# Optimization experiments

Hardware: AMD Instinct MI355X
Metric: run time of the kernel (lower is better)

The kernel has to match this reference:

```python
import jax, jax.numpy as jnp
import numpy as np

T, B, EMBED, HEADS = 1024, 32, 512, 8
HEAD = EMBED // HEADS      # per-head value size (= head_dim = 64)
KEYD = 16                  # key_size hard-coded to 16 in MultiheadAttention
MEM_SLOTS, TOPK = 8, 3
NUM_GATES = 2 * EMBED      # gate_style='unit' -> 2*mem_size


def layer_norm(x, g, b, eps=1e-5):
    mu = jnp.mean(x, axis=-1, keepdims=True)
    var = jnp.var(x, axis=-1, keepdims=True)
    return (x - mu) * jax.lax.rsqrt(var + eps) * g + b


def mha(q_src, kv_src, Wq, bq, Wk, bk, Wv, bv, use_topk):
    # q from q_src (RelationalMemory passes 'memory' arg as query source),
    # k/v from kv_src ('input' arg). No 1/sqrt(d) scaling in original code.
    Bq, Sq = q_src.shape[0], q_src.shape[1]
    Sk = kv_src.shape[1]
    q = (q_src @ Wq + bq).reshape(Bq, Sq, HEADS, KEYD)
    k = (kv_src @ Wk + bk).reshape(Bq, Sk, HEADS, KEYD)
    v = (kv_src @ Wv + bv).reshape(Bq, Sk, HEADS, HEAD)
    probs = jax.nn.softmax(jnp.einsum('bqhd,bkhd->bhqk', q, k), axis=-1)
    if use_topk:
        _, idx = jax.lax.top_k(probs, TOPK)  # (B,H,Sq,TOPK)
        mask = jnp.sum(jax.nn.one_hot(idx, Sk, dtype=probs.dtype), axis=-2)
        probs = probs * mask  # post-softmax top-k gate (scatter of ones)
    out = jnp.einsum('bhqk,bkhd->bqhd', probs, v)
    return out.reshape(Bq, Sq, EMBED)


def setup_inputs() -> dict:
    rng = jax.random.key(0)
    ks = jax.random.split(rng, 12)

    def n(k, shape, s=0.02):
        return jax.random.normal(k, shape, dtype=jnp.float32) * s

    # initial_state: eye(mem_slots) zero-padded to mem_size, per batch element
    mem0 = jnp.pad(jnp.eye(MEM_SLOTS, dtype=jnp.float32), ((0, 0), (0, EMBED - MEM_SLOTS)))
    return {
        'query': jax.random.normal(ks[0], (T, B, EMBED), jnp.float32),
        'key': jax.random.normal(ks[1], (T, B, EMBED), jnp.float32),
        'memory': jnp.tile(mem0[None], (B, 1, 1)),
        'W_in': n(ks[2], (EMBED, EMBED)), 'b_in': jnp.zeros((EMBED,), jnp.float32),
        'Wq': n(ks[3], (EMBED, KEYD * HEADS)), 'bq': jnp.zeros((KEYD * HEADS,), jnp.float32),
        'Wk': n(ks[4], (EMBED, KEYD * HEADS)), 'bk': jnp.zeros((KEYD * HEADS,), jnp.float32),
        'Wv': n(ks[5], (EMBED, EMBED)), 'bv': jnp.zeros((EMBED,), jnp.float32),
        'W_mlp': n(ks[6], (EMBED, EMBED)), 'b_mlp': jnp.zeros((EMBED,), jnp.float32),
        'g1': jnp.ones((EMBED,), jnp.float32), 'be1': jnp.zeros((EMBED,), jnp.float32),
        'g2': jnp.ones((EMBED,), jnp.float32), 'be2': jnp.zeros((EMBED,), jnp.float32),
        'w_rep': jax.random.normal(ks[7], (EMBED,), jnp.float32),
        'W_ig': n(ks[8], (EMBED, NUM_GATES)), 'b_ig': jnp.zeros((NUM_GATES,), jnp.float32),
        'W_mg': n(ks[9], (MEM_SLOTS, EMBED, NUM_GATES)), 'b_mg': jnp.zeros((MEM_SLOTS, NUM_GATES), jnp.float32),
        'forget_bias': jnp.asarray(1.0, jnp.float32),
        'input_bias': jnp.asarray(0.0, jnp.float32),
    }


def reference(query, key, memory, W_in, b_in, Wq, bq, Wk, bk, Wv, bv,
              W_mlp, b_mlp, g1, be1, g2, be2, w_rep, W_ig, b_ig,
              W_mg, b_mg, forget_bias, input_bias):
    # query only shape-checked by the torch module; key carries the content
    inputs = jnp.transpose(key, (1, 0, 2))          # (B, T, E)
    x = inputs @ W_in + b_in                        # input_projector
    # attend_over_memory (num_blocks=1): memory slots query the tokens, top-k write
    attended = mha(memory, x, Wq, bq, Wk, bk, Wv, bv, use_topk=True)
    m = layer_norm(memory + attended, g1, be1)
    mlp = jax.nn.relu(m @ W_mlp + b_mlp)            # attention_mlp_layers=1
    new_mem = layer_norm(m + mlp, g2, be2)
    # gating (gate_style='unit')
    gi = jnp.mean(jax.nn.relu(w_rep * x), axis=1) @ W_ig + b_ig      # RepeatLinear -> (B, 2E)
    gm = jnp.einsum('bsm,smn->bsn', jnp.tanh(memory), W_mg) + b_mg   # GroupLinearLayer -> (B, S, 2E)
    in_g, f_g = jnp.split(gi[:, None, :] + gm, 2, axis=-1)
    in_g = jax.nn.sigmoid(in_g + input_bias)
    f_g = jax.nn.sigmoid(f_g + forget_bias)
    new_mem = in_g * jnp.tanh(new_mem) + f_g * memory
    # broadcast read: every token queries the updated memory (no top-k)
    hx = mha(x, new_mem, Wq, bq, Wk, bk, Wv, bv, use_topk=False)     # (B, T, E)
    return jnp.transpose(hx, (1, 0, 2))             # (T, B, E) as in torch forward
```

## Files before the change

### kernel.cpp

```cpp
#include <hip/hip_runtime.h>
#include <stdint.h>

typedef unsigned short u16;
typedef __bf16 bf16x8 __attribute__((ext_vector_type(8)));
typedef float f32x4 __attribute__((ext_vector_type(4)));


__device__ __forceinline__ u16 f2b(float f) {
  union { __bf16 h; u16 u; } v; v.h = (__bf16)f; return v.u;
}
__device__ __forceinline__ float b2f(u16 h) {
  union { uint32_t u; float f; } v; v.u = ((uint32_t)h) << 16; return v.f;
}
__device__ __forceinline__ void gload_lds16(const void* g, void* l) {
  __builtin_amdgcn_global_load_lds(
      (const __attribute__((address_space(1))) unsigned int*)g,
      (__attribute__((address_space(3))) unsigned int*)l, 16, 0, 0);
}

__global__ void k_prep(const float* __restrict__ W_in, u16* __restrict__ WxT,
                       const float* __restrict__ Wv, u16* __restrict__ WvT,
                       const float* __restrict__ mem, float* __restrict__ tm,
                       const float* __restrict__ b_in, float* __restrict__ bfull,
                       const float* __restrict__ Wk, const float* __restrict__ Wq,
                       u16* __restrict__ WkqTr, u16* __restrict__ WinB,
                       const float* __restrict__ W_mlp, u16* __restrict__ WmlpT,
                       const float* __restrict__ key, u16* __restrict__ keyB) {
  int idx = blockIdx.x * 256 + threadIdx.x;
  if (idx < 262144) {
    int k = idx >> 9, n = idx & 511;
    WxT[n * 512 + k] = f2b(W_in[idx]);
  } else if (idx < 524288) {
    int j = idx - 262144;
    int k = j >> 9, n = j & 511;
    WvT[n * 512 + k] = f2b(Wv[j]);
  } else if (idx < 655360) {
    int j = idx - 524288;
    tm[j] = tanhf(mem[j]);
  } else if (idx < 655872) {
    int j = idx - 655360;
    bfull[j] = b_in[j];
  } else if (idx < 786944) {
    int i = idx - 655872;
    int j = i >> 9, n = i & 511;
    WkqTr[i] = f2b(j < 128 ? Wk[n * 128 + j] : Wq[n * 128 + j - 128]);
  } else if (idx < 1049088) {
    int i = idx - 786944;
    WinB[i] = f2b(W_in[i]);
  } else if (idx < 1311232) {
    int i = idx - 1049088;
    int k = i >> 9, n = i & 511;
    WmlpT[n * 512 + k] = f2b(W_mlp[i]);
  } else {
    int i = idx - 1311232;
    int r = i >> 6, e8 = i & 63;
    int b = r >> 10, t = r & 1023;
    const float* src = key + ((size_t)(t * 32 + b) << 9) + e8 * 8;
    float4 lo = *(const float4*)src;
    float4 hi = *(const float4*)(src + 4);
    bf16x8 o;
    o[0] = (__bf16)lo.x; o[1] = (__bf16)lo.y; o[2] = (__bf16)lo.z; o[3] = (__bf16)lo.w;
    o[4] = (__bf16)hi.x; o[5] = (__bf16)hi.y; o[6] = (__bf16)hi.z; o[7] = (__bf16)hi.w;
    *(bf16x8*)(keyB + ((size_t)r << 9) + e8 * 8) = o;
  }
}

__global__ __launch_bounds__(256) void k_wprep2(
    const u16* __restrict__ A, const u16* __restrict__ Bt, u16* __restrict__ WxT,
    const float* __restrict__ b_in, const float* __restrict__ Wk, const float* __restrict__ Wq,
    const float* __restrict__ bk, const float* __restrict__ bq, float* __restrict__ bfull,
    const float* __restrict__ memory, const float* __restrict__ bqf, float* __restrict__ qm)
{
  const int bid = blockIdx.x;
  const int tid = threadIdx.x;
  if (bid < 8) {
    __shared__ u16 As[128 * 32];
    __shared__ u16 Bs[128 * 32];
    const int m0 = (bid & 1) * 128;
    const int n0 = (bid >> 1) * 128;
    const int lane = tid & 63;
    const int wid = tid >> 6;
    const int wm = (wid >> 1) * 64;
    const int wn = (wid & 1) * 64;
    f32x4 acc[4][4];
    #pragma unroll
    for (int i = 0; i < 4; ++i)
      #pragma unroll
      for (int j = 0; j < 4; ++j) acc[i][j] = (f32x4){0.f, 0.f, 0.f, 0.f};
    for (int kt = 0; kt < 16; ++kt) {
      const int k0 = kt << 5;
      __syncthreads();
      #pragma unroll
      for (int c = 0; c < 2; ++c) {
        int o = c * 2048 + tid * 8;
        int row = o >> 5, ck = o & 31;
        gload_lds16(A + (size_t)(m0 + row) * 512 + k0 + ck, As + o);
        gload_lds16(Bt + (size_t)(n0 + row) * 512 + k0 + ck, Bs + o);
      }
      __syncthreads();
      const int r = lane & 15;
      const int kb = (lane >> 4) * 8;
      bf16x8 af[4], bfr[4];
      #pragma unroll
      for (int i = 0; i < 4; ++i) {
        af[i]  = *(const bf16x8*)(As + (wm + i * 16 + r) * 32 + kb);
        bfr[i] = *(const bf16x8*)(Bs + (wn + i * 16 + r) * 32 + kb);
      }
      #pragma unroll
      for (int i = 0; i < 4; ++i)
        #pragma unroll
        for (int j = 0; j < 4; ++j)
          acc[i][j] = __builtin_amdgcn_mfma_f32_16x16x32_bf16(af[i], bfr[j], acc[i][j], 0, 0, 0);
    }
    const int cl = lane & 15;
    const int rl = (lane >> 4) * 4;
    #pragma unroll
    for (int j = 0; j < 4; ++j) {
      const int col = n0 + wn + j * 16 + cl;
      #pragma unroll
      for (int i = 0; i < 4; ++i) {
        #pragma unroll
        for (int rr = 0; rr < 4; ++rr) {
          const int row = m0 + wm + i * 16 + rl + rr;
          WxT[(size_t)(512 + row) * 512 + col] = f2b(acc[i][j][rr]);
        }
      }
    }
  } else if (bid == 8) {
    __shared__ float bs[512];
    const int j = tid;
    bs[tid] = b_in[tid];
    bs[256 + tid] = b_in[256 + tid];
    __syncthreads();
    const float* W = (j < 128) ? (Wk + j) : (Wq + j - 128);
    float a = 0.f;
    #pragma unroll 8
    for (int n = 0; n < 512; ++n)
      a += bs[n] * W[(size_t)n * 128];
    bfull[512 + j] = a + ((j < 128) ? bk[j] : bq[j - 128]);
  } else {
    const int bs_ = bid - 9;
    const int b = bs_ >> 3, s = bs_ & 7;
    const int col = tid & 127, half = tid >> 7;
    __shared__ float mrow[512];
    __shared__ float part[2][128];
    *(float2*)&mrow[tid * 2] = *(const float2*)&memory[(size_t)(b * 8 + s) * 512 + tid * 2];
    __syncthreads();
    float a = 0.f;
    const int e0 = half * 256;
    for (int e = 0; e < 256; ++e)
      a += mrow[e0 + e] * Wq[(size_t)(e0 + e) * 128 + col];
    part[half][col] = a;
    __syncthreads();
    if (tid < 128)
      qm[(size_t)(b * 8 + s) * 128 + tid] = part[0][tid] + part[1][tid] + bqf[tid];
  }
}

__global__ __launch_bounds__(256) void gemm_xkq(
    const u16* __restrict__ keyB, const u16* __restrict__ Bt,
    const float* __restrict__ bias, u16* __restrict__ x, u16* __restrict__ kq)
{
  __shared__ u16 smem[16384];
  u16* As = smem;
  u16* Bs = smem + 8192;
  const int tid = threadIdx.x;
  const int bid = blockIdx.x;
  const int wgid = (bid & 7) * 192 + (bid >> 3);
  const int m0 = (wgid / 6) * 128;
  const int n0 = (wgid % 6) * 128;
  const int lane = tid & 63;
  const int wid = tid >> 6;
  const int wm = (wid >> 1) * 64;
  const int wn = (wid & 1) * 64;

  f32x4 acc[4][4];
  #pragma unroll
  for (int i = 0; i < 4; ++i)
    #pragma unroll
    for (int j = 0; j < 4; ++j) acc[i][j] = (f32x4){0.f, 0.f, 0.f, 0.f};

  for (int kt = 0; kt < 8; ++kt) {
    const int k0 = kt << 6;
    __syncthreads();
    #pragma unroll
    for (int c = 0; c < 4; ++c) {
      const int q = c * 256 + tid;
      const int row = q >> 3;
      const int c8 = q & 7;
      const int lc = c8 ^ (row & 7);
      gload_lds16(keyB + (size_t)(m0 + row) * 512 + k0 + lc * 8, As + q * 8);
      gload_lds16(Bt   + (size_t)(n0 + row) * 512 + k0 + lc * 8, Bs + q * 8);
    }
    __syncthreads();
    const int r = lane & 15;
    const int hi = lane >> 4;
    bf16x8 af[4][2], bfr[4][2];
    #pragma unroll
    for (int i = 0; i < 4; ++i) {
      const int ra = wm + i * 16 + r;
      const int rb = wn + i * 16 + r;
      #pragma unroll
      for (int kk = 0; kk < 2; ++kk) {
        af[i][kk]  = *(const bf16x8*)(As + ra * 64 + (((kk * 4 + hi)) ^ (ra & 7)) * 8);
        bfr[i][kk] = *(const bf16x8*)(Bs + rb * 64 + (((kk * 4 + hi)) ^ (rb & 7)) * 8);
      }
    }
    #pragma unroll
    for (int kk = 0; kk < 2; ++kk)
      #pragma unroll
      for (int i = 0; i < 4; ++i)
        #pragma unroll
        for (int j = 0; j < 4; ++j)
          acc[i][j] = __builtin_amdgcn_mfma_f32_16x16x32_bf16(af[i][kk], bfr[j][kk], acc[i][j], 0, 0, 0);
  }
  __syncthreads();
  u16* Cs = smem;
  const int cl = lane & 15;
  const int rl = (lane >> 4) * 4;
  #pragma unroll
  for (int j = 0; j < 4; ++j) {
    const int lcol = wn + j * 16 + cl;
    const float bsv = bias[n0 + lcol];
    #pragma unroll
    for (int i = 0; i < 4; ++i)
      #pragma unroll
      for (int rr = 0; rr < 4; ++rr)
        Cs[(wm + i * 16 + rl + rr) * 128 + lcol] = f2b(acc[i][j][rr] + bsv);
  }
  __syncthreads();
  #pragma unroll
  for (int c = 0; c < 8; ++c) {
    const int chunk = c * 256 + tid;
    const int row = chunk >> 4, c8 = chunk & 15;
    uint4 v = *(const uint4*)&Cs[row * 128 + c8 * 8];
    if (n0 < 512)
      *(uint4*)(x + (size_t)(m0 + row) * 512 + n0 + c8 * 8) = v;
    else
      *(uint4*)(kq + (size_t)(m0 + row) * 256 + (n0 - 512) + c8 * 8) = v;
  }
}

__global__ __launch_bounds__(256) void k_scores_topk(
    const float* __restrict__ qm, const u16* __restrict__ kq,
    const u16* __restrict__ x, float* __restrict__ p3, u16* __restrict__ XW)
{
  const int b = blockIdx.x, h = blockIdx.y, s = blockIdx.z;
  const int tid = threadIdx.x;
  __shared__ float swv[4];
  __shared__ int   swi[4];
  __shared__ float ssv[4];

  float q[16];
  const float* qp = qm + ((size_t)(b * 8 + s) * 128 + h * 16);
  #pragma unroll
  for (int d = 0; d < 16; ++d) q[d] = qp[d];

  float sc[4];
  #pragma unroll
  for (int j = 0; j < 4; ++j) {
    const int t = j * 256 + tid;
    const u16* kr = kq + ((size_t)(b * 1024 + t)) * 256 + h * 16;
    uint4 v0 = *(const uint4*)kr;
    uint4 v1 = *(const uint4*)(kr + 8);
    const u16* p0 = (const u16*)&v0;
    const u16* p1 = (const u16*)&v1;
    float a = 0.f;
    #pragma unroll
    for (int d = 0; d < 8; ++d) a += q[d] * b2f(p0[d]);
    #pragma unroll
    for (int d = 0; d < 8; ++d) a += q[8 + d] * b2f(p1[d]);
    sc[j] = a;
  }

  int   seli[3];
  float selv[3];
  float ssum = 0.f;
  #pragma unroll
  for (int pass = 0; pass < 3; ++pass) {
    float bv_ = -1e30f; int bi_ = 1 << 30;
    #pragma unroll
    for (int j = 0; j < 4; ++j) {
      const int t = j * 256 + tid;
      bool skip = false;
      for (int k = 0; k < pass; ++k) skip |= (t == seli[k]);
      float v = skip ? -1e30f : sc[j];
      if (v > bv_ || (v == bv_ && t < bi_)) { bv_ = v; bi_ = t; }
    }
    #pragma unroll
    for (int o = 32; o > 0; o >>= 1) {
      float ov = __shfl_xor(bv_, o);
      int   oi = __shfl_xor(bi_, o);
      if (ov > bv_ || (ov == bv_ && oi < bi_)) { bv_ = ov; bi_ = oi; }
    }
    __syncthreads();
    if ((tid & 63) == 0) { swv[tid >> 6] = bv_; swi[tid >> 6] = bi_; }
    __syncthreads();
    float wv = swv[0]; int wi = swi[0];
    #pragma unroll
    for (int w = 1; w < 4; ++w) {
      float ov = swv[w]; int oi = swi[w];
      if (ov > wv || (ov == wv && oi < wi)) { wv = ov; wi = oi; }
    }
    selv[pass] = wv; seli[pass] = wi;

    if (pass == 0) {
      float se = 0.f;
      #pragma unroll
      for (int j = 0; j < 4; ++j) se += __expf(sc[j] - wv);
      #pragma unroll
      for (int o = 32; o > 0; o >>= 1) se += __shfl_xor(se, o);
      __syncthreads();
      if ((tid & 63) == 0) ssv[tid >> 6] = se;
      __syncthreads();
      ssum = ssv[0] + ssv[1] + ssv[2] + ssv[3];
    }
  }

  const float m0v = selv[0];
  const float inv = 1.f / ssum;
  const float p0 = __expf(selv[0] - m0v) * inv;
  const float p1 = __expf(selv[1] - m0v) * inv;
  const float p2 = __expf(selv[2] - m0v) * inv;
  if (tid == 0) {
    const size_t base = (size_t)(b * 64 + h * 8 + s);
    p3[base * 4 + 0] = p0;
    p3[base * 4 + 1] = p1;
    p3[base * 4 + 2] = p2;
    p3[base * 4 + 3] = p0 + p1 + p2;
  }
  if (tid < 64) {
    const u16* xb = x + ((size_t)b << 19) + tid * 8;
    uint4 a0 = *(const uint4*)(xb + ((size_t)seli[0] << 9));
    uint4 a1 = *(const uint4*)(xb + ((size_t)seli[1] << 9));
    uint4 a2 = *(const uint4*)(xb + ((size_t)seli[2] << 9));
    const u16* e0 = (const u16*)&a0;
    const u16* e1 = (const u16*)&a1;
    const u16* e2 = (const u16*)&a2;
    u16 ov[8];
    #pragma unroll
    for (int k = 0; k < 8; ++k)
      ov[k] = f2b(p0 * b2f(e0[k]) + p1 * b2f(e1[k]) + p2 * b2f(e2[k]));
    *(uint4*)(XW + (size_t)h * 131072 + (size_t)(b * 8 + s) * 512 + tid * 8) = *(const uint4*)ov;
  }
}

__global__ __launch_bounds__(256) void k_attgi(
    const u16* __restrict__ XW, const u16* __restrict__ WvT,
    const float* __restrict__ p3, const float* __restrict__ bvv,
    float* __restrict__ att,
    const u16* __restrict__ x, const float* __restrict__ w_rep,
    float* __restrict__ gpart)
{
  __shared__ u16 As[128 * 32];
  __shared__ u16 Bs[64 * 32];
  __shared__ float ps[4][512];
  const int bid = blockIdx.x;
  const int tid = threadIdx.x;
  if (bid < 16) {
    const int h = bid >> 1;
    const int m0 = (bid & 1) * 128;
    const int lane = tid & 63;
    const int wid = tid >> 6;
    const int wm = wid * 32;
    const u16* A = XW + (size_t)h * 131072;
    const u16* Bh = WvT + (size_t)h * 64 * 512;

    f32x4 acc[2][4];
    #pragma unroll
    for (int i = 0; i < 2; ++i)
      #pragma unroll
      for (int j = 0; j < 4; ++j) acc[i][j] = (f32x4){0.f, 0.f, 0.f, 0.f};

    for (int kt = 0; kt < 16; ++kt) {
      const int k0 = kt << 5;
      __syncthreads();
      #pragma unroll
      for (int c = 0; c < 2; ++c) {
        int o = c * 2048 + tid * 8;
        int row = o >> 5, ck = o & 31;
        gload_lds16(A + (size_t)(m0 + row) * 512 + k0 + ck, As + o);
      }
      {
        int row = tid >> 2, ck = (tid & 3) * 8;
        gload_lds16(Bh + (size_t)row * 512 + k0 + ck, Bs + row * 32 + ck);
      }
      __syncthreads();
      const int r = lane & 15;
      const int kb = (lane >> 4) * 8;
      bf16x8 af[2], bfr[4];
      #pragma unroll
      for (int i = 0; i < 2; ++i)
        af[i] = *(const bf16x8*)(As + (wm + i * 16 + r) * 32 + kb);
      #pragma unroll
      for (int j = 0; j < 4; ++j)
        bfr[j] = *(const bf16x8*)(Bs + (j * 16 + r) * 32 + kb);
      #pragma unroll
      for (int i = 0; i < 2; ++i)
        #pragma unroll
        for (int j = 0; j < 4; ++j)
          acc[i][j] = __builtin_amdgcn_mfma_f32_16x16x32_bf16(af[i], bfr[j], acc[i][j], 0, 0, 0);
    }
    const int cl = lane & 15;
    const int rl = (lane >> 4) * 4;
    #pragma unroll
    for (int i = 0; i < 2; ++i) {
      #pragma unroll
      for (int rr = 0; rr < 4; ++rr) {
        const int row = m0 + wm + i * 16 + rl + rr;
        const int bb = row >> 3, ss = row & 7;
        const float sp = p3[(size_t)(bb * 64 + h * 8 + ss) * 4 + 3];
        #pragma unroll
        for (int j = 0; j < 4; ++j) {
          const int col = h * 64 + j * 16 + cl;
          att[(size_t)row * 512 + col] = acc[i][j][rr] + sp * bvv[col];
        }
      }
    }
  } else {
    const int j = bid - 16;
    const int b = j >> 3, ch = j & 7;
    const int e8 = tid & 63, tp = tid >> 6;
    float w[8], acc[8];
    #pragma unroll
    for (int k = 0; k < 8; ++k) { w[k] = w_rep[e8 * 8 + k]; acc[k] = 0.f; }
    const int t0 = ch * 128 + tp * 32;
    for (int tt = 0; tt < 32; ++tt) {
      uint4 v = *(const uint4*)(x + ((size_t)(b * 1024 + t0 + tt) << 9) + e8 * 8);
      const u16* pv = (const u16*)&v;
      #pragma unroll
      for (int k = 0; k < 8; ++k) acc[k] += fmaxf(w[k] * b2f(pv[k]), 0.f);
    }
    #pragma unroll
    for (int k = 0; k < 8; ++k) ps[tp][e8 * 8 + k] = acc[k];
    __syncthreads();
    #pragma unroll
    for (int r = 0; r < 2; ++r) {
      int e = r * 256 + tid;
      gpart[(size_t)(b * 8 + ch) * 512 + e] = ps[0][e] + ps[1][e] + ps[2][e] + ps[3][e];
    }
  }
}

__global__ __launch_bounds__(256) void k_ln1(
    const float* __restrict__ memory, const float* __restrict__ att,
    const float* __restrict__ g1, const float* __restrict__ be1,
    float* __restrict__ m_f32, u16* __restrict__ m_bf)
{
  const int b = blockIdx.x, s = blockIdx.y;
  const int tid = threadIdx.x;
  __shared__ float r1[256], r2[256];
  const size_t base = (size_t)(b * 8 + s) * 512;
  float v0 = memory[base + tid] + att[base + tid];
  float v1 = memory[base + 256 + tid] + att[base + 256 + tid];
  r1[tid] = v0 + v1; r2[tid] = v0 * v0 + v1 * v1;
  __syncthreads();
  for (int off = 128; off > 0; off >>= 1) {
    if (tid < off) { r1[tid] += r1[tid + off]; r2[tid] += r2[tid + off]; }
    __syncthreads();
  }
  float mu = r1[0] * (1.f / 512.f);
  float var = r2[0] * (1.f / 512.f) - mu * mu;
  float rs = rsqrtf(var + 1e-5f);
  float m0v = (v0 - mu) * rs * g1[tid] + be1[tid];
  float m1v = (v1 - mu) * rs * g1[tid + 256] + be1[tid + 256];
  m_f32[base + tid] = m0v;
  m_f32[base + 256 + tid] = m1v;
  m_bf[base + tid] = f2b(m0v);
  m_bf[base + 256 + tid] = f2b(m1v);
}

__global__ __launch_bounds__(256) void k_mlpgigm(
    const u16* __restrict__ A, const u16* __restrict__ Bt,
    const float* __restrict__ b_mlp, const float* __restrict__ m_f32,
    float* __restrict__ hbuf,
    const float* __restrict__ tm, const float* __restrict__ W_mg, float* __restrict__ gmp,
    const float* __restrict__ gpart, const float* __restrict__ W_ig,
    const float* __restrict__ b_ig, float* __restrict__ gip)
{
  __shared__ __align__(16) char smem[73728];
  const int bid = blockIdx.x;
  const int tid = threadIdx.x;
  if (bid < 8) {
    u16* As = (u16*)smem;
    u16* Bs = (u16*)(smem + 16384);
    const int m0 = (bid >> 2) * 128;
    const int n0 = (bid & 3) * 128;
    const int lane = tid & 63;
    const int wid = tid >> 6;
    const int wm = (wid >> 1) * 64;
    const int wn = (wid & 1) * 64;

    f32x4 acc[4][4];
    #pragma unroll
    for (int i = 0; i < 4; ++i)
      #pragma unroll
      for (int j = 0; j < 4; ++j) acc[i][j] = (f32x4){0.f, 0.f, 0.f, 0.f};

    for (int kt = 0; kt < 8; ++kt) {
      const int k0 = kt << 6;
      __syncthreads();
      #pragma unroll
      for (int c = 0; c < 4; ++c) {
        const int q = c * 256 + tid;
        const int row = q >> 3;
        const int c8 = q & 7;
        const int lc = c8 ^ (row & 7);
        gload_lds16(A  + (size_t)(m0 + row) * 512 + k0 + lc * 8, As + q * 8);
        gload_lds16(Bt + (size_t)(n0 + row) * 512 + k0 + lc * 8, Bs + q * 8);
      }
      __syncthreads();
      const int r = lane & 15;
      const int hi = lane >> 4;
      bf16x8 af[4][2], bfr[4][2];
      #pragma unroll
      for (int i = 0; i < 4; ++i) {
        const int ra = wm + i * 16 + r;
        const int rb = wn + i * 16 + r;
        #pragma unroll
        for (int kk = 0; kk < 2; ++kk) {
          af[i][kk]  = *(const bf16x8*)(As + ra * 64 + (((kk * 4 + hi)) ^ (ra & 7)) * 8);
          bfr[i][kk] = *(const bf16x8*)(Bs + rb * 64 + (((kk * 4 + hi)) ^ (rb & 7)) * 8);
        }
      }
      #pragma unroll
      for (int kk = 0; kk < 2; ++kk)
        #pragma unroll
        for (int i = 0; i < 4; ++i)
          #pragma unroll
          for (int j = 0; j < 4; ++j)
            acc[i][j] = __builtin_amdgcn_mfma_f32_16x16x32_bf16(af[i][kk], bfr[j][kk], acc[i][j], 0, 0, 0);
    }
    const int cl = lane & 15;
    const int rl = (lane >> 4) * 4;
    #pragma unroll
    for (int j = 0; j < 4; ++j) {
      const int col = n0 + wn + j * 16 + cl;
      const float bsv = b_mlp[col];
      #pragma unroll
      for (int i = 0; i < 4; ++i) {
        #pragma unroll
        for (int rr = 0; rr < 4; ++rr) {
          const int row = m0 + wm + i * 16 + rl + rr;
          hbuf[(size_t)row * 512 + col] = m_f32[(size_t)row * 512 + col] + fmaxf(acc[i][j][rr] + bsv, 0.f);
        }
      }
    }
  } else if (bid < 264) {
    float* wtile = (float*)smem;
    float* vals  = (float*)(smem + 65536);
    const int g = bid - 8;
    const int s = g >> 5, nc = (g >> 3) & 3, kc = g & 7;
    const int k0 = kc * 64;
    const float* wsrc = W_mg + (size_t)s * 524288 + (size_t)k0 * 1024 + nc * 256;
    #pragma unroll
    for (int i = 0; i < 16; ++i) {
      const int q = i * 256 + tid;
      const int row = q >> 6, c16 = q & 63;
      gload_lds16(wsrc + (size_t)row * 1024 + c16 * 4, wtile + q * 4);
    }
    {
      int i = tid * 2;
      int b = i >> 4, k4 = i & 15;
      *(float4*)&vals[b * 64 + k4 * 4] = *(const float4*)&tm[(size_t)(b * 8 + s) * 512 + k0 + k4 * 4];
      i++;
      b = i >> 4; k4 = i & 15;
      *(float4*)&vals[b * 64 + k4 * 4] = *(const float4*)&tm[(size_t)(b * 8 + s) * 512 + k0 + k4 * 4];
    }
    __syncthreads();
    const int col = nc * 256 + tid;
    float acc[32];
    #pragma unroll
    for (int b = 0; b < 32; ++b) acc[b] = 0.f;
    for (int kk = 0; kk < 64; ++kk) {
      float w = wtile[kk * 256 + tid];
      #pragma unroll
      for (int b = 0; b < 32; ++b) acc[b] += vals[b * 64 + kk] * w;
    }
    #pragma unroll
    for (int b = 0; b < 32; ++b)
      gmp[(size_t)((kc * 32 + b) * 8 + s) * 1024 + col] = acc[b];
  } else {
    float* wtile = (float*)smem;
    float* vals  = (float*)(smem + 65536);
    const int j = bid - 264;
    const int nc = j >> 3, kc = j & 7;
    const int k0 = kc * 64;
    const float* wsrc = W_ig + (size_t)k0 * 1024 + nc * 256;
    #pragma unroll
    for (int i = 0; i < 16; ++i) {
      const int q = i * 256 + tid;
      const int row = q >> 6, c16 = q & 63;
      gload_lds16(wsrc + (size_t)row * 1024 + c16 * 4, wtile + q * 4);
    }
    #pragma unroll
    for (int i = 0; i < 8; ++i) {
      const int idx = i * 256 + tid;
      const int b = idx >> 6, k = idx & 63;
      float a = 0.f;
      #pragma unroll
      for (int ch = 0; ch < 8; ++ch)
        a += gpart[(size_t)(b * 8 + ch) * 512 + k0 + k];
      vals[b * 64 + k] = a * (1.f / 1024.f);
    }
    __syncthreads();
    const int col = nc * 256 + tid;
    float acc[32];
    #pragma unroll
    for (int b = 0; b < 32; ++b) acc[b] = 0.f;
    for (int kk = 0; kk < 64; ++kk) {
      float w = wtile[kk * 256 + tid];
      #pragma unroll
      for (int b = 0; b < 32; ++b) acc[b] += vals[b * 64 + kk] * w;
    }
    const float badd = (kc == 0) ? b_ig[col] : 0.f;
    #pragma unroll
    for (int b = 0; b < 32; ++b)
      gip[(size_t)(kc * 32 + b) * 1024 + col] = acc[b] + badd;
  }
}

__global__ __launch_bounds__(256) void k_ln2gate(
    const float* __restrict__ hbuf, const float* __restrict__ g2, const float* __restrict__ be2,
    const float* __restrict__ gip, const float* __restrict__ gmp,
    const float* __restrict__ b_mg, const float* __restrict__ memory,
    const float* __restrict__ fbias, const float* __restrict__ ibias,
    float* __restrict__ nmem)
{
  const int b = blockIdx.x, s = blockIdx.y;
  const int tid = threadIdx.x;
  __shared__ float r1[256], r2[256];
  const size_t base = (size_t)(b * 8 + s) * 512;
  float v0 = hbuf[base + tid];
  float v1 = hbuf[base + 256 + tid];
  r1[tid] = v0 + v1; r2[tid] = v0 * v0 + v1 * v1;
  __syncthreads();
  for (int off = 128; off > 0; off >>= 1) {
    if (tid < off) { r1[tid] += r1[tid + off]; r2[tid] += r2[tid + off]; }
    __syncthreads();
  }
  float mu = r1[0] * (1.f / 512.f);
  float var = r2[0] * (1.f / 512.f) - mu * mu;
  float rs = rsqrtf(var + 1e-5f);
  const float fb = fbias[0], ib = ibias[0];
  #pragma unroll
  for (int rr = 0; rr < 2; ++rr) {
    const int e = rr * 256 + tid;
    const float v = (rr == 0) ? v0 : v1;
    float ln = (v - mu) * rs * g2[e] + be2[e];
    float gin = b_mg[s * 1024 + e], gfn = b_mg[s * 1024 + 512 + e];
    #pragma unroll
    for (int kc = 0; kc < 8; ++kc) {
      size_t gp = (size_t)((kc * 32 + b) * 8 + s) * 1024;
      gin += gmp[gp + e];
      gfn += gmp[gp + 512 + e];
    }
    float giv_i = 0.f, giv_f = 0.f;
    #pragma unroll
    for (int kc = 0; kc < 8; ++kc) {
      size_t gp = (size_t)(kc * 32 + b) * 1024;
      giv_i += gip[gp + e];
      giv_f += gip[gp + 512 + e];
    }
    float ing = 1.f / (1.f + __expf(-(giv_i + gin + ib)));
    float fg  = 1.f / (1.f + __expf(-(giv_f + gfn + fb)));
    nmem[base + e] = ing * tanhf(ln) + fg * memory[base + e];
  }
}

__global__ __launch_bounds__(256) void k_kv_part(
    const float* __restrict__ nmem, const float* __restrict__ Wk, const float* __restrict__ Wv,
    float* __restrict__ kvp)
{
  const int b = blockIdx.x, nc = blockIdx.y, kc = blockIdx.z;
  const int tid = threadIdx.x;
  const int col = tid & 127, rg = tid >> 7;
  const int k0 = kc * 128;
  __shared__ float nm[8][128];
  {
    int s = tid >> 5, k4 = tid & 31;
    *(float4*)&nm[s][k4 * 4] = *(const float4*)&nmem[(size_t)(b * 8 + s) * 512 + k0 + k4 * 4];
  }
  __syncthreads();
  const int cg = nc * 128 + col;
  const float* wp; int stride;
  if (nc == 0) { wp = Wk + (size_t)k0 * 128 + cg; stride = 128; }
  else         { wp = Wv + (size_t)k0 * 512 + (cg - 128); stride = 512; }
  const int b0 = rg * 4;
  float a0 = 0.f, a1 = 0.f, a2 = 0.f, a3 = 0.f;
  #pragma unroll 4
  for (int kk = 0; kk < 128; ++kk) {
    float w = wp[(size_t)kk * stride];
    a0 += nm[b0][kk] * w;
    a1 += nm[b0 + 1][kk] * w;
    a2 += nm[b0 + 2][kk] * w;
    a3 += nm[b0 + 3][kk] * w;
  }
  kvp[(size_t)((kc * 32 + b) * 8 + b0    ) * 640 + cg] = a0;
  kvp[(size_t)((kc * 32 + b) * 8 + b0 + 1) * 640 + cg] = a1;
  kvp[(size_t)((kc * 32 + b) * 8 + b0 + 2) * 640 + cg] = a2;
  kvp[(size_t)((kc * 32 + b) * 8 + b0 + 3) * 640 + cg] = a3;
}

__global__ __launch_bounds__(256) void k_out_attn(
    const u16* __restrict__ kq, const float* __restrict__ kvp,
    const float* __restrict__ bk, const float* __restrict__ bv,
    float* __restrict__ out)
{
  int b = blockIdx.x, tc = blockIdx.y;
  int tid = threadIdx.x;
  __shared__ float km[1024];
  __shared__ float vm[4096];
  __shared__ float pr[1024];
  for (int i = tid; i < 1024; i += 256) {
    int s = i >> 7, j = i & 127;
    float a = bk[j];
    #pragma unroll
    for (int kc = 0; kc < 4; ++kc)
      a += kvp[(size_t)((kc * 32 + b) * 8 + s) * 640 + j];
    km[i] = a;
  }
  for (int i = tid; i < 4096; i += 256) {
    int s = i >> 9, c = i & 511;
    float a = bv[c];
    #pragma unroll
    for (int kc = 0; kc < 4; ++kc)
      a += kvp[(size_t)((kc * 32 + b) * 8 + s) * 640 + 128 + c];
    vm[i] = a;
  }
  __syncthreads();
  if (tid < 128) {
    int tt = tid >> 3, hh = tid & 7;
    int t = tc * 16 + tt;
    const u16* qrow = kq + ((size_t)(b * 1024 + t)) * 256 + 128 + hh * 16;
    float q[16];
    #pragma unroll
    for (int d = 0; d < 16; ++d) q[d] = b2f(qrow[d]);
    float s8[8]; float mx = -1e38f;
    #pragma unroll
    for (int s = 0; s < 8; ++s) {
      float a = 0.f;
      #pragma unroll
      for (int d = 0; d < 16; ++d) a += q[d] * km[s * 128 + hh * 16 + d];
      s8[s] = a; mx = fmaxf(mx, a);
    }
    float se = 0.f;
    #pragma unroll
    for (int s = 0; s < 8; ++s) { s8[s] = __expf(s8[s] - mx); se += s8[s]; }
    float inv = 1.f / se;
    #pragma unroll
    for (int s = 0; s < 8; ++s) pr[(tt * 8 + hh) * 8 + s] = s8[s] * inv;
  }
  __syncthreads();
  #pragma unroll
  for (int oi = 0; oi < 8; ++oi) {
    int o = oi * 256 + tid;
    int tt = o >> 7, c4 = o & 127;
    int c = c4 * 4, hh = c >> 6;
    const float* prp = &pr[(tt * 8 + hh) * 8];
    float4 r = {0.f, 0.f, 0.f, 0.f};
    #pragma unroll
    for (int s = 0; s < 8; ++s) {
      float p = prp[s];
      float4 v = *(const float4*)&vm[s * 512 + c];
      r.x += p * v.x; r.y += p * v.y; r.z += p * v.z; r.w += p * v.w;
    }
    int t = tc * 16 + tt;
    *(float4*)&out[((size_t)t * 32 + b) * 512 + c] = r;
  }
}

extern "C" void kernel_launch(void* const* d_in, const int* in_sizes, int n_in,
                              void* d_out, int out_size, void* d_ws, size_t ws_size,
                              hipStream_t stream) {
  (void)in_sizes; (void)n_in; (void)out_size; (void)ws_size;
  const float* key   = (const float*)d_in[1];
  const float* memory= (const float*)d_in[2];
  const float* W_in  = (const float*)d_in[3];
  const float* b_in  = (const float*)d_in[4];
  const float* Wq    = (const float*)d_in[5];
  const float* bq    = (const float*)d_in[6];
  const float* Wk    = (const float*)d_in[7];
  const float* bk    = (const float*)d_in[8];
  const float* Wv    = (const float*)d_in[9];
  const float* bv    = (const float*)d_in[10];
  const float* W_mlp = (const float*)d_in[11];
  const float* b_mlp = (const float*)d_in[12];
  const float* g1    = (const float*)d_in[13];
  const float* be1   = (const float*)d_in[14];
  const float* g2    = (const float*)d_in[15];
  const float* be2   = (const float*)d_in[16];
  const float* w_rep = (const float*)d_in[17];
  const float* W_ig  = (const float*)d_in[18];
  const float* b_ig  = (const float*)d_in[19];
  const float* W_mg  = (const float*)d_in[20];
  const float* b_mg  = (const float*)d_in[21];
  const float* fbias = (const float*)d_in[22];
  const float* ibias = (const float*)d_in[23];
  float* out = (float*)d_out;

  char* p = (char*)d_ws;
  auto alloc = [&](size_t bytes) { char* r = p; p += (bytes + 255) & ~(size_t)255; return r; };
  u16* x       = (u16*)alloc(33554432);
  u16* keyB    = (u16*)alloc(33554432);
  u16* kq      = (u16*)alloc(16777216);
  u16* WxT     = (u16*)alloc(786432);
  u16* WvT     = (u16*)alloc(524288);
  u16* WkqTr   = (u16*)alloc(262144);
  u16* WinB    = (u16*)alloc(524288);
  u16* WmlpT   = (u16*)alloc(524288);
  float* bfull = (float*)alloc(3072);
  float* gpart = (float*)alloc(524288);
  float* gip   = (float*)alloc(1048576);
  float* gmp   = (float*)alloc(8388608);
  float* att   = (float*)alloc(524288);
  float* m_f32 = (float*)alloc(524288);
  u16*   m_bf  = (u16*)alloc(262144);
  float* hbuf  = (float*)alloc(524288);
  float* nmem  = (float*)alloc(524288);
  float* kvp   = (float*)alloc(2621440);
  float* tm    = (float*)alloc(524288);
  float* qmw   = (float*)alloc(131072);
  float* p3    = (float*)alloc(32768);
  u16* XW      = (u16*)alloc(2097152);

  k_prep<<<13314, 256, 0, stream>>>(W_in, WxT, Wv, WvT, memory, tm, b_in, bfull,
                                    Wk, Wq, WkqTr, WinB, W_mlp, WmlpT, key, keyB);
  k_wprep2<<<265, 256, 0, stream>>>(WkqTr, WinB, WxT, b_in, Wk, Wq, bk, bq, bfull,
                                    memory, bq, qmw);
  gemm_xkq<<<1536, 256, 0, stream>>>(keyB, WxT, bfull, x, kq);
  k_scores_topk<<<dim3(32, 8, 8), 256, 0, stream>>>(qmw, kq, x, p3, XW);
  k_attgi<<<272, 256, 0, stream>>>(XW, WvT, p3, bv, att, x, w_rep, gpart);
  k_ln1<<<dim3(32, 8), 256, 0, stream>>>(memory, att, g1, be1, m_f32, m_bf);
  k_mlpgigm<<<296, 256, 0, stream>>>(m_bf, WmlpT, b_mlp, m_f32, hbuf,
                                     tm, W_mg, gmp, gpart, W_ig, b_ig, gip);
  k_ln2gate<<<dim3(32, 8), 256, 0, stream>>>(hbuf, g2, be2, gip, gmp, b_mg, memory,
                                             fbias, ibias, nmem);
  k_kv_part<<<dim3(32, 5, 4), 256, 0, stream>>>(nmem, Wk, Wv, kvp);
  k_out_attn<<<dim3(32, 64), 256, 0, stream>>>(kq, kvp, bk, bv, out);
}
```

Before: 170.1 us.

## Fuse LN2/gating into KV projection and move small prep work into prep kernel

The bias-fold and memory-query blocks move out of the weight-combine kernel and into the big prep kernel as extra blocks, so the combine GEMM becomes its own 8-block kernel. The LN2 plus gating kernel is merged into the K/V partial-projection kernel: each block recomputes layer-norm stats for its batch and the gated memory slice it needs, so the nmem round trip and one launch go away. In exchange, the gating work is done redundantly across the 5 column chunks of each (batch, k-chunk) pair.

Result: slower. 177.4 us (+4.3%).

```diff
diff --git a/kernel.cpp b/kernel.cpp
--- a/kernel.cpp
+++ b/kernel.cpp
@@ -25,135 +25,138 @@
                        const float* __restrict__ Wk, const float* __restrict__ Wq,
                        u16* __restrict__ WkqTr, u16* __restrict__ WinB,
                        const float* __restrict__ W_mlp, u16* __restrict__ WmlpT,
-                       const float* __restrict__ key, u16* __restrict__ keyB) {
-  int idx = blockIdx.x * 256 + threadIdx.x;
-  if (idx < 262144) {
-    int k = idx >> 9, n = idx & 511;
-    WxT[n * 512 + k] = f2b(W_in[idx]);
-  } else if (idx < 524288) {
-    int j = idx - 262144;
-    int k = j >> 9, n = j & 511;
-    WvT[n * 512 + k] = f2b(Wv[j]);
-  } else if (idx < 655360) {
-    int j = idx - 524288;
-    tm[j] = tanhf(mem[j]);
-  } else if (idx < 655872) {
-    int j = idx - 655360;
-    bfull[j] = b_in[j];
-  } else if (idx < 786944) {
-    int i = idx - 655872;
-    int j = i >> 9, n = i & 511;
-    WkqTr[i] = f2b(j < 128 ? Wk[n * 128 + j] : Wq[n * 128 + j - 128]);
-  } else if (idx < 1049088) {
-    int i = idx - 786944;
-    WinB[i] = f2b(W_in[i]);
-  } else if (idx < 1311232) {
-    int i = idx - 1049088;
-    int k = i >> 9, n = i & 511;
-    WmlpT[n * 512 + k] = f2b(W_mlp[i]);
+                       const float* __restrict__ key, u16* __restrict__ keyB,
+                       const float* __restrict__ bk, const float* __restrict__ bq,
+                       float* __restrict__ qm) {
+  __shared__ float sh_a[512];
+  __shared__ float sh_p[2][128];
+  const int tid = threadIdx.x;
+  if (blockIdx.x < 13314) {
+    int idx = blockIdx.x * 256 + tid;
+    if (idx < 262144) {
+      int k = idx >> 9, n = idx & 511;
+      WxT[n * 512 + k] = f2b(W_in[idx]);
+    } else if (idx < 524288) {
+      int j = idx - 262144;
+      int k = j >> 9, n = j & 511;
+      WvT[n * 512 + k] = f2b(Wv[j]);
+    } else if (idx < 655360) {
+      int j = idx - 524288;
+      tm[j] = tanhf(mem[j]);
+    } else if (idx < 655872) {
+      int j = idx - 655360;
+      bfull[j] = b_in[j];
+    } else if (idx < 786944) {
+      int i = idx - 655872;
+      int j = i >> 9, n = i & 511;
+      WkqTr[i] = f2b(j < 128 ? Wk[n * 128 + j] : Wq[n * 128 + j - 128]);
+    } else if (idx < 1049088) {
+      int i = idx - 786944;
+      WinB[i] = f2b(W_in[i]);
+    } else if (idx < 1311232) {
+      int i = idx - 1049088;
+      int k = i >> 9, n = i & 511;
+      WmlpT[n * 512 + k] = f2b(W_mlp[i]);
+    } else {
+      int i = idx - 1311232;
+      int r = i >> 6, e8 = i & 63;
+      int b = r >> 10, t = r & 1023;
+      const float* src = key + ((size_t)(t * 32 + b) << 9) + e8 * 8;
+      float4 lo = *(const float4*)src;
+      float4 hi = *(const float4*)(src + 4);
+      bf16x8 o;
+      o[0] = (__bf16)lo.x; o[1] = (__bf16)lo.y; o[2] = (__bf16)lo.z; o[3] = (__bf16)lo.w;
+      o[4] = (__bf16)hi.x; o[5] = (__bf16)hi.y; o[6] = (__bf16)hi.z; o[7] = (__bf16)hi.w;
+      *(bf16x8*)(keyB + ((size_t)r << 9) + e8 * 8) = o;
+    }
   } else {
-    int i = idx - 1311232;
-    int r = i >> 6, e8 = i & 63;
-    int b = r >> 10, t = r & 1023;
-    const float* src = key + ((size_t)(t * 32 + b) << 9) + e8 * 8;
-    float4 lo = *(const float4*)src;
-    float4 hi = *(const float4*)(src + 4);
-    bf16x8 o;
-    o[0] = (__bf16)lo.x; o[1] = (__bf16)lo.y; o[2] = (__bf16)lo.z; o[3] = (__bf16)lo.w;
-    o[4] = (__bf16)hi.x; o[5] = (__bf16)hi.y; o[6] = (__bf16)hi.z; o[7] = (__bf16)hi.w;
-    *(bf16x8*)(keyB + ((size_t)r << 9) + e8 * 8) = o;
-  }
-}
-
-__global__ __launch_bounds__(256) void k_wprep2(
-    const u16* __restrict__ A, const u16* __restrict__ Bt, u16* __restrict__ WxT,
-    const float* __restrict__ b_in, const float* __restrict__ Wk, const float* __restrict__ Wq,
-    const float* __restrict__ bk, const float* __restrict__ bq, float* __restrict__ bfull,
-    const float* __restrict__ memory, const float* __restrict__ bqf, float* __restrict__ qm)
+    const int wb = blockIdx.x - 13314;
+    if (wb == 0) {
+      sh_a[tid] = b_in[tid];
+      sh_a[256 + tid] = b_in[256 + tid];
+      __syncthreads();
+      const int j = tid;
+      const float* W = (j < 128) ? (Wk + j) : (Wq + j - 128);
+      float a = 0.f;
+      #pragma unroll 8
+      for (int n = 0; n < 512; ++n)
+        a += sh_a[n] * W[(size_t)n * 128];
+      bfull[512 + j] = a + ((j < 128) ? bk[j] : bq[j - 128]);
+    } else {
+      const int bs_ = wb - 1;
+      const int b = bs_ >> 3, s = bs_ & 7;
+      const int col = tid & 127, half = tid >> 7;
+      *(float2*)&sh_a[tid * 2] = *(const float2*)&mem[(size_t)(b * 8 + s) * 512 + tid * 2];
+      __syncthreads();
+      float a = 0.f;
+      const int e0 = half * 256;
+      for (int e = 0; e < 256; ++e)
+        a += sh_a[e0 + e] * Wq[(size_t)(e0 + e) * 128 + col];
+      sh_p[half][col] = a;
+      __syncthreads();
+      if (tid < 128)
+        qm[(size_t)(b * 8 + s) * 128 + tid] = sh_p[0][tid] + sh_p[1][tid] + bq[tid];
+    }
+  }
+}
+
+__global__ __launch_bounds__(256) void gemm_wc(
+    const u16* __restrict__ A, const u16* __restrict__ Bt, u16* __restrict__ WxT)
 {
-  const int bid = blockIdx.x;
+  __shared__ u16 As[128 * 32];
+  __shared__ u16 Bs[128 * 32];
   const int tid = threadIdx.x;
-  if (bid < 8) {
-    __shared__ u16 As[128 * 32];
-    __shared__ u16 Bs[128 * 32];
-    const int m0 = (bid & 1) * 128;
-    const int n0 = (bid >> 1) * 128;
-    const int lane = tid & 63;
-    const int wid = tid >> 6;
-    const int wm = (wid >> 1) * 64;
-    const int wn = (wid & 1) * 64;
-    f32x4 acc[4][4];
+  const int m0 = blockIdx.x * 128;
+  const int n0 = blockIdx.y * 128;
+  const int lane = tid & 63;
+  const int wid = tid >> 6;
+  const int wm = (wid >> 1) * 64;
+  const int wn = (wid & 1) * 64;
+
+  f32x4 acc[4][4];
+  #pragma unroll
+  for (int i = 0; i < 4; ++i)
+    #pragma unroll
+    for (int j = 0; j < 4; ++j) acc[i][j] = (f32x4){0.f, 0.f, 0.f, 0.f};
+
+  for (int kt = 0; kt < 16; ++kt) {
+    const int k0 = kt << 5;
+    __syncthreads();
+    #pragma unroll
+    for (int c = 0; c < 2; ++c) {
+      int o = c * 2048 + tid * 8;
+      int row = o >> 5, ck = o & 31;
+      gload_lds16(A + (size_t)(m0 + row) * 512 + k0 + ck, As + o);
+      gload_lds16(Bt + (size_t)(n0 + row) * 512 + k0 + ck, Bs + o);
+    }
+    __syncthreads();
+    const int r = lane & 15;
+    const int kb = (lane >> 4) * 8;
+    bf16x8 af[4], bfr[4];
+    #pragma unroll
+    for (int i = 0; i < 4; ++i) {
+      af[i]  = *(const bf16x8*)(As + (wm + i * 16 + r) * 32 + kb);
+      bfr[i] = *(const bf16x8*)(Bs + (wn + i * 16 + r) * 32 + kb);
+    }
     #pragma unroll
     for (int i = 0; i < 4; ++i)
       #pragma unroll
-      for (int j = 0; j < 4; ++j) acc[i][j] = (f32x4){0.f, 0.f, 0.f, 0.f};
-    for (int kt = 0; kt < 16; ++kt) {
-      const int k0 = kt << 5;
-      __syncthreads();
-      #pragma unroll
-      for (int c = 0; c < 2; ++c) {
-        int o = c * 2048 + tid * 8;
-        int row = o >> 5, ck = o & 31;
-        gload_lds16(A + (size_t)(m0 + row) * 512 + k0 + ck, As + o);
-        gload_lds16(Bt + (size_t)(n0 + row) * 512 + k0 + ck, Bs + o);
+      for (int j = 0; j < 4; ++j)
+        acc[i][j] = __builtin_amdgcn_mfma_f32_16x16x32_bf16(af[i], bfr[j], acc[i][j], 0, 0, 0);
+  }
+  const int cl = lane & 15;
+  const int rl = (lane >> 4) * 4;
+  #pragma unroll
+  for (int j = 0; j < 4; ++j) {
+    const int col = n0 + wn + j * 16 + cl;
+    #pragma unroll
+    for (int i = 0; i < 4; ++i) {
+      #pragma unroll
+      for (int rr = 0; rr < 4; ++rr) {
+        const int row = m0 + wm + i * 16 + rl + rr;
+        WxT[(size_t)(512 + row) * 512 + col] = f2b(acc[i][j][rr]);
       }
-      __syncthreads();
-      const int r = lane & 15;
-      const int kb = (lane >> 4) * 8;
-      bf16x8 af[4], bfr[4];
-      #pragma unroll
-      for (int i = 0; i < 4; ++i) {
-        af[i]  = *(const bf16x8*)(As + (wm + i * 16 + r) * 32 + kb);
-        bfr[i] = *(const bf16x8*)(Bs + (wn + i * 16 + r) * 32 + kb);
-      }
-      #pragma unroll
-      for (int i = 0; i < 4; ++i)
-        #pragma unroll
-        for (int j = 0; j < 4; ++j)
-          acc[i][j] = __builtin_amdgcn_mfma_f32_16x16x32_bf16(af[i], bfr[j], acc[i][j], 0, 0, 0);
-    }
-    const int cl = lane & 15;
-    const int rl = (lane >> 4) * 4;
-    #pragma unroll
-    for (int j = 0; j < 4; ++j) {
-      const int col = n0 + wn + j * 16 + cl;
-      #pragma unroll
-      for (int i = 0; i < 4; ++i) {
-        #pragma unroll
-        for (int rr = 0; rr < 4; ++rr) {
-          const int row = m0 + wm + i * 16 + rl + rr;
-          WxT[(size_t)(512 + row) * 512 + col] = f2b(acc[i][j][rr]);
-        }
-      }
-    }
-  } else if (bid == 8) {
-    __shared__ float bs[512];
-    const int j = tid;
-    bs[tid] = b_in[tid];
-    bs[256 + tid] = b_in[256 + tid];
-    __syncthreads();
-    const float* W = (j < 128) ? (Wk + j) : (Wq + j - 128);
-    float a = 0.f;
-    #pragma unroll 8
-    for (int n = 0; n < 512; ++n)
-      a += bs[n] * W[(size_t)n * 128];
-    bfull[512 + j] = a + ((j < 128) ? bk[j] : bq[j - 128]);
-  } else {
-    const int bs_ = bid - 9;
-    const int b = bs_ >> 3, s = bs_ & 7;
-    const int col = tid & 127, half = tid >> 7;
-    __shared__ float mrow[512];
-    __shared__ float part[2][128];
-    *(float2*)&mrow[tid * 2] = *(const float2*)&memory[(size_t)(b * 8 + s) * 512 + tid * 2];
-    __syncthreads();
-    float a = 0.f;
-    const int e0 = half * 256;
-    for (int e = 0; e < 256; ++e)
-      a += mrow[e0 + e] * Wq[(size_t)(e0 + e) * 128 + col];
-    part[half][col] = a;
-    __syncthreads();
-    if (tid < 128)
-      qm[(size_t)(b * 8 + s) * 128 + tid] = part[0][tid] + part[1][tid] + bqf[tid];
+    }
   }
 }
 
@@ -620,68 +623,76 @@
   }
 }
 
-__global__ __launch_bounds__(256) void k_ln2gate(
+__global__ __launch_bounds__(256) void k_kvgate(
     const float* __restrict__ hbuf, const float* __restrict__ g2, const float* __restrict__ be2,
     const float* __restrict__ gip, const float* __restrict__ gmp,
     const float* __restrict__ b_mg, const float* __restrict__ memory,
     const float* __restrict__ fbias, const float* __restrict__ ibias,
-    float* __restrict__ nmem)
-{
-  const int b = blockIdx.x, s = blockIdx.y;
-  const int tid = threadIdx.x;
-  __shared__ float r1[256], r2[256];
-  const size_t base = (size_t)(b * 8 + s) * 512;
-  float v0 = hbuf[base + tid];
-  float v1 = hbuf[base + 256 + tid];
-  r1[tid] = v0 + v1; r2[tid] = v0 * v0 + v1 * v1;
-  __syncthreads();
-  for (int off = 128; off > 0; off >>= 1) {
-    if (tid < off) { r1[tid] += r1[tid + off]; r2[tid] += r2[tid + off]; }
-    __syncthreads();
-  }
-  float mu = r1[0] * (1.f / 512.f);
-  float var = r2[0] * (1.f / 512.f) - mu * mu;
-  float rs = rsqrtf(var + 1e-5f);
-  const float fb = fbias[0], ib = ibias[0];
-  #pragma unroll
-  for (int rr = 0; rr < 2; ++rr) {
-    const int e = rr * 256 + tid;
-    const float v = (rr == 0) ? v0 : v1;
-    float ln = (v - mu) * rs * g2[e] + be2[e];
-    float gin = b_mg[s * 1024 + e], gfn = b_mg[s * 1024 + 512 + e];
-    #pragma unroll
-    for (int kc = 0; kc < 8; ++kc) {
-      size_t gp = (size_t)((kc * 32 + b) * 8 + s) * 1024;
-      gin += gmp[gp + e];
-      gfn += gmp[gp + 512 + e];
-    }
-    float giv_i = 0.f, giv_f = 0.f;
-    #pragma unroll
-    for (int kc = 0; kc < 8; ++kc) {
-      size_t gp = (size_t)(kc * 32 + b) * 1024;
-      giv_i += gip[gp + e];
-      giv_f += gip[gp + 512 + e];
-    }
-    float ing = 1.f / (1.f + __expf(-(giv_i + gin + ib)));
-    float fg  = 1.f / (1.f + __expf(-(giv_f + gfn + fb)));
-    nmem[base + e] = ing * tanhf(ln) + fg * memory[base + e];
-  }
-}
-
-__global__ __launch_bounds__(256) void k_kv_part(
-    const float* __restrict__ nmem, const float* __restrict__ Wk, const float* __restrict__ Wv,
+    const float* __restrict__ Wk, const float* __restrict__ Wv,
     float* __restrict__ kvp)
 {
   const int b = blockIdx.x, nc = blockIdx.y, kc = blockIdx.z;
   const int tid = threadIdx.x;
+  const int k0 = kc * 128;
+  __shared__ float hb[8][512];
+  __shared__ float red[2][8][32];
+  __shared__ float mus[8], rss[8];
+  __shared__ float nm[8][128];
+  #pragma unroll
+  for (int i = 0; i < 4; ++i) {
+    int idx = i * 256 + tid;
+    int s = idx >> 7, c4 = idx & 127;
+    *(float4*)&hb[s][c4 * 4] = *(const float4*)&hbuf[(size_t)(b * 8 + s) * 512 + c4 * 4];
+  }
+  __syncthreads();
+  {
+    int s = tid >> 5, l = tid & 31;
+    float sm = 0.f, sq = 0.f;
+    #pragma unroll
+    for (int j = 0; j < 16; ++j) {
+      float v = hb[s][l * 16 + j];
+      sm += v; sq += v * v;
+    }
+    red[0][s][l] = sm; red[1][s][l] = sq;
+  }
+  __syncthreads();
+  if (tid < 8) {
+    float sm = 0.f, sq = 0.f;
+    #pragma unroll
+    for (int l = 0; l < 32; ++l) { sm += red[0][tid][l]; sq += red[1][tid][l]; }
+    float mu = sm * (1.f / 512.f);
+    float var = sq * (1.f / 512.f) - mu * mu;
+    mus[tid] = mu;
+    rss[tid] = rsqrtf(var + 1e-5f);
+  }
+  __syncthreads();
+  const float fb = fbias[0], ib = ibias[0];
+  #pragma unroll
+  for (int i = 0; i < 4; ++i) {
+    int idx = i * 256 + tid;
+    int s = idx >> 7, ee = idx & 127;
+    int e = k0 + ee;
+    float ln = (hb[s][e] - mus[s]) * rss[s] * g2[e] + be2[e];
+    float gin = b_mg[s * 1024 + e], gfn = b_mg[s * 1024 + 512 + e];
+    #pragma unroll
+    for (int kc2 = 0; kc2 < 8; ++kc2) {
+      size_t gp = (size_t)((kc2 * 32 + b) * 8 + s) * 1024;
+      gin += gmp[gp + e];
+      gfn += gmp[gp + 512 + e];
+    }
+    float giv_i = 0.f, giv_f = 0.f;
+    #pragma unroll
+    for (int kc2 = 0; kc2 < 8; ++kc2) {
+      size_t gp = (size_t)(kc2 * 32 + b) * 1024;
+      giv_i += gip[gp + e];
+      giv_f += gip[gp + 512 + e];
+    }
+    float ing = 1.f / (1.f + __expf(-(giv_i + gin + ib)));
+    float fg  = 1.f / (1.f + __expf(-(giv_f + gfn + fb)));
+    nm[s][ee] = ing * tanhf(ln) + fg * memory[(size_t)(b * 8 + s) * 512 + e];
+  }
+  __syncthreads();
   const int col = tid & 127, rg = tid >> 7;
-  const int k0 = kc * 128;
-  __shared__ float nm[8][128];
-  {
-    int s = tid >> 5, k4 = tid & 31;
-    *(float4*)&nm[s][k4 * 4] = *(const float4*)&nmem[(size_t)(b * 8 + s) * 512 + k0 + k4 * 4];
-  }
-  __syncthreads();
   const int cg = nc * 128 + col;
   const float* wp; int stride;
   if (nc == 0) { wp = Wk + (size_t)k0 * 128 + cg; stride = 128; }
@@ -817,25 +828,23 @@
   float* m_f32 = (float*)alloc(524288);
   u16*   m_bf  = (u16*)alloc(262144);
   float* hbuf  = (float*)alloc(524288);
-  float* nmem  = (float*)alloc(524288);
   float* kvp   = (float*)alloc(2621440);
   float* tm    = (float*)alloc(524288);
   float* qmw   = (float*)alloc(131072);
   float* p3    = (float*)alloc(32768);
   u16* XW      = (u16*)alloc(2097152);
 
-  k_prep<<<13314, 256, 0, stream>>>(W_in, WxT, Wv, WvT, memory, tm, b_in, bfull,
-                                    Wk, Wq, WkqTr, WinB, W_mlp, WmlpT, key, keyB);
-  k_wprep2<<<265, 256, 0, stream>>>(WkqTr, WinB, WxT, b_in, Wk, Wq, bk, bq, bfull,
-                                    memory, bq, qmw);
+  k_prep<<<13571, 256, 0, stream>>>(W_in, WxT, Wv, WvT, memory, tm, b_in, bfull,
+                                    Wk, Wq, WkqTr, WinB, W_mlp, WmlpT, key, keyB,
+                                    bk, bq, qmw);
+  gemm_wc<<<dim3(2, 4), 256, 0, stream>>>(WkqTr, WinB, WxT);
   gemm_xkq<<<1536, 256, 0, stream>>>(keyB, WxT, bfull, x, kq);
   k_scores_topk<<<dim3(32, 8, 8), 256, 0, stream>>>(qmw, kq, x, p3, XW);
   k_attgi<<<272, 256, 0, stream>>>(XW, WvT, p3, bv, att, x, w_rep, gpart);
   k_ln1<<<dim3(32, 8), 256, 0, stream>>>(memory, att, g1, be1, m_f32, m_bf);
   k_mlpgigm<<<296, 256, 0, stream>>>(m_bf, WmlpT, b_mlp, m_f32, hbuf,
                                      tm, W_mg, gmp, gpart, W_ig, b_ig, gip);
-  k_ln2gate<<<dim3(32, 8), 256, 0, stream>>>(hbuf, g2, be2, gip, gmp, b_mg, memory,
-                                             fbias, ibias, nmem);
-  k_kv_part<<<dim3(32, 5, 4), 256, 0, stream>>>(nmem, Wk, Wv, kvp);
+  k_kvgate<<<dim3(32, 5, 4), 256, 0, stream>>>(hbuf, g2, be2, gip, gmp, b_mg, memory,
+                                               fbias, ibias, Wk, Wv, kvp);
   k_out_attn<<<dim3(32, 64), 256, 0, stream>>>(kq, kvp, bk, bv, out);
 }
```
